# Optimization experiments

Hardware: AMD Instinct MI355X
Metric: run time of the kernel (lower is better)

## Reference

```python
import jax, jax.numpy as jnp
import numpy as np

B, T, C, H, N_LAYER, LAYER_ID = 4, 2048, 1024, 16, 12, 6
N = C // H
Q = 256  # T % 256 == 0 -> chunk size used by the module


def setup_inputs():
    key = jax.random.key(0)
    ks = jax.random.split(key, 9)
    r0 = LAYER_ID / (N_LAYER - 1)
    r1 = 1.0 - LAYER_ID / N_LAYER
    ddd = (jnp.arange(C, dtype=jnp.float32) / C)[None, None, :]
    h = jnp.arange(C, dtype=jnp.float32)
    s = 1.0 / np.sqrt(C)
    return {
        "x": jax.random.normal(ks[0], (B, T, C), jnp.float32),
        "time_maa_x": 1.0 - ddd ** r1,
        "time_maa_w": 1.0 - ddd ** r1,
        "time_maa_k": 1.0 - ddd ** r1,
        "time_maa_v": 1.0 - (ddd ** r1 + 0.3 * r0),
        "time_maa_r": 1.0 - ddd ** (0.5 * r1),
        "maa_w1": jax.random.uniform(ks[1], (C, 4 * 32), jnp.float32, minval=-0.01, maxval=0.01),
        "maa_w2": jax.random.uniform(ks[2], (4, 32, C), jnp.float32, minval=-0.01, maxval=0.01),
        "decay_w1": jax.random.uniform(ks[3], (C, 64), jnp.float32, minval=-0.01, maxval=0.01),
        "decay_w2": jax.random.uniform(ks[4], (64, C), jnp.float32, minval=-0.01, maxval=0.01),
        "time_decay": (-6.0 + 5.0 * (h / (C - 1)) ** (0.7 + 1.3 * r0))[None, None, :],
        "time_faaaa": (r0 * (1.0 - h / (C - 1))).reshape(1, H, 1, 1, N),
        "Wr": jax.random.normal(ks[5], (C, C), jnp.float32) * s,
        "Wk": jax.random.normal(ks[6], (C, C), jnp.float32) * s,
        "Wv": jax.random.normal(ks[7], (C, C), jnp.float32) * s,
        "Wo": jax.random.normal(ks[8], (C, C), jnp.float32) * s,
        "ln_g": jnp.ones((C,), jnp.float32),
        "ln_b": jnp.zeros((C,), jnp.float32),
    }


def _forward(x, time_maa_x, time_maa_w, time_maa_k, time_maa_v, time_maa_r,
             maa_w1, maa_w2, decay_w1, decay_w2, time_decay, time_faaaa,
             Wr, Wk, Wv, Wo, ln_g, ln_b):
    b, t, c = x.shape
    nc = t // Q
    # time_shift: zero-pad one step at front of time axis, drop last step
    xx = jnp.pad(x, ((0, 0), (1, 0), (0, 0)))[:, :-1] - x
    xxx = x + xx * time_maa_x
    m = jnp.tanh(xxx @ maa_w1).reshape(b, t, 4, -1)  # [B,T,4,32]
    m = jnp.einsum('btfd,fdc->fbtc', m, maa_w2)       # [4,B,T,C]
    mw, mk, mv, mr = m[0], m[1], m[2], m[3]
    xw = x + xx * (time_maa_w + mw)
    xk = x + xx * (time_maa_k + mk)
    xv = x + xx * (time_maa_v + mv)
    xr = x + xx * (time_maa_r + mr)
    r = (xr @ Wr).reshape(b, t, H, N).transpose(0, 2, 1, 3)  # [B,H,T,N]
    k = (xk @ Wk).reshape(b, t, H, N).transpose(0, 2, 1, 3)
    v = (xv @ Wv).reshape(b, t, H, N).transpose(0, 2, 1, 3)
    w = time_decay + jnp.tanh(xw @ decay_w1) @ decay_w2      # [B,T,C]
    w = w.reshape(b, t, H, N).transpose(0, 2, 1, 3).mean(axis=-1)  # [B,H,T]
    w_log = -jnp.exp(w)
    wc = w_log.reshape(b, H, nc, Q, 1)
    wc_cum = jnp.cumsum(wc, axis=-2)
    shifted = jnp.pad(wc_cum, ((0, 0), (0, 0), (0, 0), (1, 0), (0, 0)))[..., :-1, :]
    ws_log = wc.sum(axis=-2, keepdims=True)   # [B,H,nc,1,1]
    w_inter = jnp.exp(ws_log - wc_cum)        # [B,H,nc,Q,1]
    w_intra = jnp.exp(wc_cum - wc)            # [B,H,nc,Q,1]
    ws = jnp.exp(ws_log)                      # [B,H,nc,1,1]
    A = shifted - jnp.swapaxes(wc_cum, -1, -2)  # [B,H,nc,Q,Q]
    strict = jnp.tril(jnp.ones((Q, Q), dtype=bool), -1)
    # torch: tril() -> exp() -> tril(-1)  ==  exp on strict-lower, zero elsewhere
    w_mask = jnp.where(strict, jnp.exp(jnp.where(strict, A, 0.0)), 0.0)
    rr = r.reshape(b, H, nc, Q, N)
    kk = k.reshape(b, H, nc, Q, N)
    vv = v.reshape(b, H, nc, Q, N)
    kv = jnp.einsum('bhcqn,bhcqm->bhcnm', kk * w_inter, vv)  # [B,H,nc,N,N]

    def step(state, inp):
        ws_i, kv_i = inp
        return ws_i * state + kv_i, state  # emit state BEFORE update (as in torch loop)

    _, states = jax.lax.scan(step, jnp.zeros((b, H, N, N), x.dtype),
                             (jnp.moveaxis(ws, 2, 0), jnp.moveaxis(kv, 2, 0)))
    states = jnp.moveaxis(states, 0, 2)  # [B,H,nc,N,N]
    inter = jnp.einsum('bhcqn,bhcnm->bhcqm', rr * w_intra, states)
    scores = jnp.einsum('bhcqn,bhckn->bhcqk', rr, kk) * w_mask
    diag = jnp.sum(rr * (time_faaaa * kk), axis=-1)  # [B,H,nc,Q]
    intra = jnp.einsum('bhcqk,bhckm->bhcqm', scores, vv) + diag[..., None] * vv
    y = (inter + intra).reshape(b, H, t, N).transpose(0, 2, 1, 3).reshape(b, t, c)
    mu = y.mean(axis=-1, keepdims=True)
    var = ((y - mu) ** 2).mean(axis=-1, keepdims=True)
    y = (y - mu) / jnp.sqrt(var + 1e-5) * ln_g + ln_b  # ln_x
    return y @ Wo  # output projection (dropout p=0)


def reference(x, time_maa_x, time_maa_w, time_maa_k, time_maa_v, time_maa_r,
              maa_w1, maa_w2, decay_w1, decay_w2, time_decay, time_faaaa,
              Wr, Wk, Wv, Wo, ln_g, ln_b):
    return _forward(x, time_maa_x, time_maa_w, time_maa_k, time_maa_v, time_maa_r,
                    maa_w1, maa_w2, decay_w1, decay_w2, time_decay, time_faaaa,
                    Wr, Wk, Wv, Wo, ln_g, ln_b)
```

## Files before the change

### kernel.cpp

```cpp
#include <hip/hip_runtime.h>
#include <math.h>

#define BB 4
#define TT 2048
#define CC 1024
#define HH 16
#define NN 64
#define QQ 256
#define NCH 8
#define BT 8192

typedef unsigned short u16;
typedef __attribute__((ext_vector_type(8))) short bf16x8;
typedef __attribute__((ext_vector_type(4))) short bf16x4;
typedef __attribute__((ext_vector_type(4))) float f32x4;
typedef __attribute__((ext_vector_type(4))) u16 u16x4;

__device__ inline u16 f2b(float x) {
  union { float f; unsigned u; } v;
  v.f = x;
  unsigned r = v.u + 0x7FFFu + ((v.u >> 16) & 1u);
  return (u16)(r >> 16);
}
__device__ inline float b2f(u16 u) {
  union { unsigned u; float f; } v;
  v.u = ((unsigned)u) << 16;
  return v.f;
}
__device__ inline bf16x8 ldfrag(const u16* p) {
  bf16x4 lo = *(const bf16x4*)p;
  bf16x4 hi = *(const bf16x4*)(p + 4);
  return __builtin_shufflevector(lo, hi, 0, 1, 2, 3, 4, 5, 6, 7);
}
__device__ inline void stage_tile(const u16* __restrict__ g, size_t base,
                                  int pitch, int tid, u16* __restrict__ lds) {
#pragma unroll
  for (int it = 0; it < 2; it++) {
    int cidx = tid + it * 256;
    int r = cidx >> 3, c8 = (cidx & 7) * 8;
    bf16x8 v = *(const bf16x8*)(g + base + (size_t)r * pitch + c8);
    *(bf16x4*)(lds + r * 72 + c8) = __builtin_shufflevector(v, v, 0, 1, 2, 3);
    *(bf16x4*)(lds + r * 72 + c8 + 4) = __builtin_shufflevector(v, v, 4, 5, 6, 7);
  }
}

__global__ __launch_bounds__(256) void mix_kernel(const float* __restrict__ x,
                                                  const float* __restrict__ tmx,
                                                  u16* __restrict__ xxxb) {
  size_t e = ((size_t)blockIdx.x * 256 + threadIdx.x) * 4;
  int c = (int)(e & 1023);
  size_t row = e >> 10;
  int t = (int)(row & 2047);
  float4 xv = *(const float4*)(x + e);
  float4 pv = make_float4(0.f, 0.f, 0.f, 0.f);
  if (t > 0) pv = *(const float4*)(x + e - 1024);
  float4 d = make_float4(pv.x - xv.x, pv.y - xv.y, pv.z - xv.z, pv.w - xv.w);
  u16x4 o;
  o.x = f2b(xv.x + d.x * tmx[c + 0]);
  o.y = f2b(xv.y + d.y * tmx[c + 1]);
  o.z = f2b(xv.z + d.z * tmx[c + 2]);
  o.w = f2b(xv.w + d.w * tmx[c + 3]);
  *(u16x4*)(xxxb + e) = o;
}

__global__ __launch_bounds__(256) void cvt_wT(const float* __restrict__ W0,
                                              const float* __restrict__ W1,
                                              const float* __restrict__ W2,
                                              const float* __restrict__ W3,
                                              u16* __restrict__ O0,
                                              u16* __restrict__ O1,
                                              u16* __restrict__ O2,
                                              u16* __restrict__ O3) {
  const float* W;
  u16* O;
  switch (blockIdx.z) {
    case 0: W = W0; O = O0; break;
    case 1: W = W1; O = O1; break;
    case 2: W = W2; O = O2; break;
    default: W = W3; O = O3; break;
  }
  __shared__ float t[64][65];
  int bx = blockIdx.x * 64;
  int by = blockIdx.y * 64;
#pragma unroll
  for (int it = 0; it < 16; it++) {
    int idx = it * 256 + threadIdx.x;
    int r = idx >> 6, c = idx & 63;
    t[r][c] = W[(size_t)(by + r) * 1024 + bx + c];
  }
  __syncthreads();
#pragma unroll
  for (int it = 0; it < 16; it++) {
    int idx = it * 256 + threadIdx.x;
    int n = idx >> 6, k = idx & 63;
    O[(size_t)(bx + n) * 1024 + by + k] = f2b(t[k][n]);
  }
}

__global__ __launch_bounds__(256) void cvt3_T(const float* __restrict__ w1,
                                              const float* __restrict__ w2,
                                              const float* __restrict__ d1,
                                              u16* __restrict__ o1,
                                              u16* __restrict__ o2,
                                              u16* __restrict__ o3,
                                              const float* __restrict__ dw2,
                                              const float* __restrict__ td,
                                              float* __restrict__ dw2r,
                                              float* __restrict__ tdr,
                                              u16* __restrict__ dw2rbT) {
  if (blockIdx.z == 3) {
    if (blockIdx.y != 0 || blockIdx.x >= 4) return;
    int idx = blockIdx.x * 256 + threadIdx.x;
    if (idx < 1024) {
      int j = idx >> 4, h = idx & 15;
      float s = 0.f;
      for (int n = 0; n < 64; n++) s += dw2[(size_t)j * 1024 + h * 64 + n];
      float m = s * (1.f / 64.f);
      dw2r[j * 16 + h] = m;
      dw2rbT[h * 64 + j] = f2b(m);
    }
    if (idx < 16) {
      float s = 0.f;
      for (int n = 0; n < 64; n++) s += td[idx * 64 + n];
      tdr[idx] = s * (1.f / 64.f);
    }
    return;
  }
  const float* in;
  u16* out;
  int R, C;
  switch (blockIdx.z) {
    case 0: in = w1; out = o1; R = 1024; C = 128; break;
    case 1: in = w2; out = o2; R = 128; C = 1024; break;
    default: in = d1; out = o3; R = 1024; C = 64; break;
  }
  int c0 = blockIdx.x * 64, r0 = blockIdx.y * 64;
  if (c0 >= C || r0 >= R) return;
  __shared__ float t[64][65];
#pragma unroll
  for (int it = 0; it < 16; it++) {
    int idx = it * 256 + threadIdx.x;
    int r = idx >> 6, c = idx & 63;
    t[r][c] = in[(size_t)(r0 + r) * C + c0 + c];
  }
  __syncthreads();
#pragma unroll
  for (int it = 0; it < 16; it++) {
    int idx = it * 256 + threadIdx.x;
    int c = idx >> 6, r = idx & 63;
    out[(size_t)(c0 + c) * R + r0 + r] = f2b(t[r][c]);
  }
}

__global__ __launch_bounds__(256) void gemm_maa(const u16* __restrict__ A,
                                                const u16* __restrict__ Bt,
                                                u16* __restrict__ Cb) {
  __shared__ u16 As[64 * 32];
  __shared__ u16 Bs[64 * 32];
  const int tid = threadIdx.x;
  const int lane = tid & 63;
  const int wave = tid >> 6;
  const int wc = wave * 16;
  const int fr = lane & 15;
  const int fq = lane >> 4;
  const int row0 = blockIdx.y * 64;
  const int col0 = blockIdx.x * 64;

  f32x4 acc[4];
#pragma unroll
  for (int i = 0; i < 4; i++) acc[i] = (f32x4){0.f, 0.f, 0.f, 0.f};

  const int ra = tid >> 2, ca = (tid & 3) * 8;

  for (int k0 = 0; k0 < 1024; k0 += 32) {
    __builtin_amdgcn_global_load_lds(
        (const __attribute__((address_space(1))) void*)(A + (size_t)(row0 + ra) * 1024 + k0 + ca),
        (__attribute__((address_space(3))) void*)(As + tid * 8), 16, 0, 0);
    __builtin_amdgcn_global_load_lds(
        (const __attribute__((address_space(1))) void*)(Bt + (size_t)(col0 + ra) * 1024 + k0 + ca),
        (__attribute__((address_space(3))) void*)(Bs + tid * 8), 16, 0, 0);
    __syncthreads();
    bf16x8 bf = *(const bf16x8*)(Bs + ((wc + fr) * 32 + fq * 8));
#pragma unroll
    for (int i = 0; i < 4; i++) {
      bf16x8 af = *(const bf16x8*)(As + ((i * 16 + fr) * 32 + fq * 8));
      acc[i] = __builtin_amdgcn_mfma_f32_16x16x32_bf16(af, bf, acc[i], 0, 0, 0);
    }
    __syncthreads();
  }
#pragma unroll
  for (int i = 0; i < 4; i++) {
    int grow = row0 + i * 16 + fq * 4;
#pragma unroll
    for (int r = 0; r < 4; r++)
      Cb[(size_t)(grow + r) * 128 + col0 + wc + fr] = f2b(tanhf(acc[i][r]));
  }
}

#define DP_ABUF 8192
#define DP_BBUF 16384
#define DP_SBUF 24576
#define DP_SMEM_BYTES 147456

template <bool TRIPLE, bool F32OUT>
__global__ __launch_bounds__(512, 2) void gemm_dp(
    const u16* __restrict__ A0, const u16* __restrict__ A1,
    const u16* __restrict__ A2, const u16* __restrict__ B0,
    const u16* __restrict__ B1, const u16* __restrict__ B2,
    float* __restrict__ Cf, u16* __restrict__ C0, u16* __restrict__ C1,
    u16* __restrict__ C2) {
  extern __shared__ __align__(16) u16 smem[];
  const int nwg = (int)(gridDim.x * gridDim.y * gridDim.z);
  const int wg = (int)(blockIdx.x + (blockIdx.y << 2) + (blockIdx.z << 8));
  const int cpx = nwg >> 3;
  const int swz = (wg & 7) * cpx + (wg >> 3);
  const int bx = swz & 3;
  const int by = (swz >> 2) & 63;
  const int bz = swz >> 8;

  const u16* __restrict__ A;
  const u16* __restrict__ Bt;
  u16* __restrict__ Cb;
  if (TRIPLE) {
    switch (bz) {
      case 0: A = A0; Bt = B0; Cb = C0; break;
      case 1: A = A1; Bt = B1; Cb = C1; break;
      default: A = A2; Bt = B2; Cb = C2; break;
    }
  } else {
    A = A0; Bt = B0; Cb = C0;
  }

  const int tid = threadIdx.x;
  const int lane = tid & 63;
  const int wave = tid >> 6;
  const int wr = (wave >> 2) * 64;
  const int wc = (wave & 3) * 64;
  const int fr = lane & 15;
  const int fq = lane >> 4;
  const int s8 = fr & 7;
  const int row0 = by * 128;
  const int col0 = bx * 256;

  int aoff[4][2], boff[4][2];
#pragma unroll
  for (int mi = 0; mi < 4; mi++)
#pragma unroll
    for (int ks = 0; ks < 2; ks++)
      aoff[mi][ks] = (wr + mi * 16 + fr) * 64 + (((ks * 4 + fq) ^ s8) * 8);
#pragma unroll
  for (int nj = 0; nj < 4; nj++)
#pragma unroll
    for (int ks = 0; ks < 2; ks++)
      boff[nj][ks] = (wc + nj * 16 + fr) * 64 + (((ks * 4 + fq) ^ s8) * 8);

  auto stage = [&](int kt, int q) {
    const u16* __restrict__ gA = A + (size_t)row0 * 1024 + kt * 64;
    const u16* __restrict__ gB = Bt + (size_t)col0 * 1024 + kt * 64;
    u16* dA = smem + q * DP_SBUF;
    u16* dB = dA + DP_ABUF;
#pragma unroll
    for (int p = 0; p < 2; p++) {
      int pos = tid + p * 512;
      int r = pos >> 3, gch = (pos & 7) ^ (r & 7);
      __builtin_amdgcn_global_load_lds(
          (const __attribute__((address_space(1))) void*)(gA + (size_t)r * 1024 + gch * 8),
          (__attribute__((address_space(3))) void*)(dA + pos * 8), 16, 0, 0);
    }
#pragma unroll
    for (int p = 0; p < 4; p++) {
      int pos = tid + p * 512;
      int r = pos >> 3, gch = (pos & 7) ^ (r & 7);
      __builtin_amdgcn_global_load_lds(
          (const __attribute__((address_space(1))) void*)(gB + (size_t)r * 1024 + gch * 8),
          (__attribute__((address_space(3))) void*)(dB + pos * 8), 16, 0, 0);
    }
  };

  f32x4 acc[4][4];
#pragma unroll
  for (int mi = 0; mi < 4; mi++)
#pragma unroll
    for (int nj = 0; nj < 4; nj++) acc[mi][nj] = (f32x4){0.f, 0.f, 0.f, 0.f};

  auto iter_body = [&](int qc, int qs, bool dostage, int t2) {
    if (dostage) stage(t2, qs);
    const u16* sA = smem + qc * DP_SBUF;
    const u16* sB = sA + DP_ABUF;
    bf16x8 av[4][2], bv[4][2];
#pragma unroll
    for (int mi = 0; mi < 4; mi++)
#pragma unroll
      for (int ks = 0; ks < 2; ks++)
        av[mi][ks] = *(const bf16x8*)(sA + aoff[mi][ks]);
#pragma unroll
    for (int nj = 0; nj < 4; nj++)
#pragma unroll
      for (int ks = 0; ks < 2; ks++)
        bv[nj][ks] = *(const bf16x8*)(sB + boff[nj][ks]);
    __builtin_amdgcn_s_setprio(1);
#pragma unroll
    for (int ks = 0; ks < 2; ks++)
#pragma unroll
      for (int mi = 0; mi < 4; mi++)
#pragma unroll
        for (int nj = 0; nj < 4; nj++)
          acc[mi][nj] = __builtin_amdgcn_mfma_f32_16x16x32_bf16(
              av[mi][ks], bv[nj][ks], acc[mi][nj], 0, 0, 0);
    __builtin_amdgcn_s_setprio(0);
  };

  stage(0, 0);
  stage(1, 1);
  int qc = 0, qs = 2;
  for (int t = 0; t < 14; t++) {
    asm volatile("s_waitcnt vmcnt(6)" ::: "memory");
    __builtin_amdgcn_s_barrier();
    iter_body(qc, qs, true, t + 2);
    qc = (qc == 2) ? 0 : qc + 1;
    qs = (qs == 2) ? 0 : qs + 1;
  }
  asm volatile("s_waitcnt vmcnt(6)" ::: "memory");
  __builtin_amdgcn_s_barrier();
  iter_body(qc, 0, false, 0);
  qc = (qc == 2) ? 0 : qc + 1;
  asm volatile("s_waitcnt vmcnt(0)" ::: "memory");
  __builtin_amdgcn_s_barrier();
  iter_body(qc, 0, false, 0);

#pragma unroll
  for (int mi = 0; mi < 4; mi++) {
    int grow = row0 + wr + mi * 16 + fq * 4;
#pragma unroll
    for (int nj = 0; nj < 4; nj++) {
      int gcol = col0 + wc + nj * 16 + fr;
#pragma unroll
      for (int r = 0; r < 4; r++) {
        if (F32OUT)
          Cf[(size_t)(grow + r) * 1024 + gcol] = acc[mi][nj][r];
        else
          Cb[(size_t)(grow + r) * 1024 + gcol] = f2b(acc[mi][nj][r]);
      }
    }
  }
}

__global__ __launch_bounds__(256) void blend_mfma(
    const u16* __restrict__ mb, const u16* __restrict__ w2T,
    const float* __restrict__ x,
    const float* __restrict__ tmw, const float* __restrict__ tmk,
    const float* __restrict__ tmv, const float* __restrict__ tmr,
    u16* __restrict__ xwb, u16* __restrict__ xkb, u16* __restrict__ xvb,
    u16* __restrict__ xrb) {
  __shared__ u16 mS[64 * 136];
  __shared__ u16 wS[64 * 136];
  const int tid = threadIdx.x;
  const int lane = tid & 63;
  const int w = tid >> 6;
  const int fr = lane & 15;
  const int fq = lane >> 4;
  const int c0 = blockIdx.x * 64;
  const int bt0 = blockIdx.y * 64;

#pragma unroll
  for (int it = 0; it < 4; it++) {
    int idx = tid + it * 256;
    int r = idx >> 4, c8 = (idx & 15) * 8;
    bf16x8 v = *(const bf16x8*)(mb + (size_t)(bt0 + r) * 128 + c8);
    *(bf16x4*)(mS + r * 136 + c8) = __builtin_shufflevector(v, v, 0, 1, 2, 3);
    *(bf16x4*)(mS + r * 136 + c8 + 4) = __builtin_shufflevector(v, v, 4, 5, 6, 7);
    bf16x8 u = *(const bf16x8*)(w2T + (size_t)(c0 + r) * 128 + c8);
    *(bf16x4*)(wS + r * 136 + c8) = __builtin_shufflevector(u, u, 0, 1, 2, 3);
    *(bf16x4*)(wS + r * 136 + c8 + 4) = __builtin_shufflevector(u, u, 4, 5, 6, 7);
  }
  __syncthreads();

  f32x4 acc[4][4];
#pragma unroll
  for (int j = 0; j < 4; j++)
#pragma unroll
    for (int f = 0; f < 4; f++) acc[j][f] = (f32x4){0.f, 0.f, 0.f, 0.f};

#pragma unroll
  for (int f = 0; f < 4; f++) {
    bf16x8 aA = ldfrag(mS + (w * 16 + fr) * 136 + f * 32 + fq * 8);
#pragma unroll
    for (int j = 0; j < 4; j++) {
      bf16x8 bB = ldfrag(wS + (j * 16 + fr) * 136 + f * 32 + fq * 8);
      acc[j][f] = __builtin_amdgcn_mfma_f32_16x16x32_bf16(aA, bB, acc[j][f], 0, 0, 0);
    }
  }

#pragma unroll
  for (int j = 0; j < 4; j++) {
    int c = c0 + j * 16 + fr;
    float w_ = tmw[c], k_ = tmk[c], v_ = tmv[c], r_ = tmr[c];
#pragma unroll
    for (int rr = 0; rr < 4; rr++) {
      int bt = bt0 + w * 16 + fq * 4 + rr;
      size_t g = (size_t)bt * 1024 + c;
      float xv_ = x[g];
      float xp = ((bt & 2047) != 0) ? x[g - 1024] : 0.f;
      float dx = xp - xv_;
      xwb[g] = f2b(xv_ + dx * (w_ + acc[j][0][rr]));
      xkb[g] = f2b(xv_ + dx * (k_ + acc[j][1][rr]));
      xvb[g] = f2b(xv_ + dx * (v_ + acc[j][2][rr]));
      xrb[g] = f2b(xv_ + dx * (r_ + acc[j][3][rr]));
    }
  }
}

__global__ __launch_bounds__(256) void decay_mfma(const u16* __restrict__ xwb,
                                                  const u16* __restrict__ d1T,
                                                  const u16* __restrict__ dw2rbT,
                                                  const float* __restrict__ tdr,
                                                  float* __restrict__ wlog) {
  __shared__ u16 As[64 * 32];
  __shared__ u16 Bs[64 * 32];
  __shared__ u16 h1S[64 * 72];
  __shared__ u16 dwS[16 * 72];
  const int tid = threadIdx.x;
  const int lane = tid & 63;
  const int w = tid >> 6;
  const int fr = lane & 15;
  const int fq = lane >> 4;
  const int bt0 = blockIdx.x * 64;

#pragma unroll
  for (int it = 0; it < 4; it++) {
    int idx = tid + it * 256;
    int r = idx >> 6, c = idx & 63;
    dwS[r * 72 + c] = dw2rbT[r * 64 + c];
  }

  f32x4 acc[4];
#pragma unroll
  for (int j = 0; j < 4; j++) acc[j] = (f32x4){0.f, 0.f, 0.f, 0.f};

  const int ra = tid >> 2, ca = (tid & 3) * 8;
  for (int k0 = 0; k0 < 1024; k0 += 32) {
    __builtin_amdgcn_global_load_lds(
        (const __attribute__((address_space(1))) void*)(xwb + (size_t)(bt0 + ra) * 1024 + k0 + ca),
        (__attribute__((address_space(3))) void*)(As + tid * 8), 16, 0, 0);
    __builtin_amdgcn_global_load_lds(
        (const __attribute__((address_space(1))) void*)(d1T + (size_t)ra * 1024 + k0 + ca),
        (__attribute__((address_space(3))) void*)(Bs + tid * 8), 16, 0, 0);
    __syncthreads();
    bf16x8 aA = *(const bf16x8*)(As + ((w * 16 + fr) * 32 + fq * 8));
#pragma unroll
    for (int j = 0; j < 4; j++) {
      bf16x8 bB = *(const bf16x8*)(Bs + ((j * 16 + fr) * 32 + fq * 8));
      acc[j] = __builtin_amdgcn_mfma_f32_16x16x32_bf16(aA, bB, acc[j], 0, 0, 0);
    }
    __syncthreads();
  }
#pragma unroll
  for (int j = 0; j < 4; j++)
#pragma unroll
    for (int rr = 0; rr < 4; rr++)
      h1S[(w * 16 + fq * 4 + rr) * 72 + j * 16 + fr] = f2b(tanhf(acc[j][rr]));
  __syncthreads();

  f32x4 a2 = (f32x4){0.f, 0.f, 0.f, 0.f};
#pragma unroll
  for (int ks = 0; ks < 2; ks++) {
    bf16x8 aA = ldfrag(h1S + (w * 16 + fr) * 72 + ks * 32 + fq * 8);
    bf16x8 bB = ldfrag(dwS + fr * 72 + ks * 32 + fq * 8);
    a2 = __builtin_amdgcn_mfma_f32_16x16x32_bf16(aA, bB, a2, 0, 0, 0);
  }
  float tdv = tdr[fr];
#pragma unroll
  for (int rr = 0; rr < 4; rr++) {
    int bt = bt0 + w * 16 + fq * 4 + rr;
    int b = bt >> 11, tl = bt & 2047;
    wlog[((size_t)(b * 16 + fr)) * 2048 + tl] = -__expf(tdv + a2[rr]);
  }
}

__global__ __launch_bounds__(256) void wprep_kernel(const float* __restrict__ wlog,
                                                    float* __restrict__ cum,
                                                    float* __restrict__ excl,
                                                    float* __restrict__ wsl) {
  int bid = blockIdx.x;
  int c = bid & 7, bh = bid >> 3;
  int q = threadIdx.x;
  float v = wlog[(size_t)bh * 2048 + c * 256 + q];
  __shared__ float s[256];
  s[q] = v;
  float val = v;
  for (int off = 1; off < 256; off <<= 1) {
    __syncthreads();
    float t = (q >= off) ? s[q - off] : 0.f;
    __syncthreads();
    val += t;
    s[q] = val;
  }
  __syncthreads();
  float total = s[255];
  cum[(size_t)bid * 256 + q] = val;
  excl[(size_t)bid * 256 + q] = val - v;
  if (q == 0) wsl[bid] = total;
}

__global__ __launch_bounds__(256) void kvfuse_kernel(
    const u16* __restrict__ vb, const u16* __restrict__ kb,
    const u16* __restrict__ rb, const float* __restrict__ faaaa,
    const float* __restrict__ cum, const float* __restrict__ wsl,
    u16* __restrict__ vT, float* __restrict__ diagG, float* __restrict__ kvb) {
  int bid = blockIdx.x;
  int c = bid & 7, bh = bid >> 3;
  int b = bh >> 4, h = bh & 15;
  __shared__ float tv[64][65];
  __shared__ float tk[64][65];
  __shared__ u16 kSb[64 * 72];
  __shared__ u16 vSb[64 * 72];
  __shared__ float wfacS[256];
  __shared__ float faS[64];
  const int tid = threadIdx.x;
  const int lane = tid & 63;
  const int w = tid >> 6;
  const int fr = lane & 15;
  const int fq = lane >> 4;
  const int m = lane;

  float wslog = wsl[bid];
  wfacS[tid] = __expf(wslog - cum[(size_t)bid * 256 + tid]);
  if (tid < 64) faS[tid] = faaaa[h * 64 + tid];

  f32x4 acc[4];
#pragma unroll
  for (int j = 0; j < 4; j++) acc[j] = (f32x4){0.f, 0.f, 0.f, 0.f};

  for (int qt = 0; qt < 4; qt++) {
    __syncthreads();
    float fam = faS[m];
    int t0 = c * QQ + qt * 64;
#pragma unroll
    for (int it = 0; it < 16; it++) {
      int r = it * 4 + w;
      size_t g = ((size_t)(b * TT + t0 + r)) * CC + h * 64 + m;
      float vraw = b2f(vb[g]);
      float kraw = b2f(kb[g]);
      float rraw = b2f(rb[g]);
      tv[r][m] = vraw;
      tk[r][m] = kraw;
      float s = rraw * fam * kraw;
      s += __shfl_xor(s, 1);
      s += __shfl_xor(s, 2);
      s += __shfl_xor(s, 4);
      s += __shfl_xor(s, 8);
      s += __shfl_xor(s, 16);
      s += __shfl_xor(s, 32);
      if (m == 0) diagG[(size_t)bh * 2048 + t0 + r] = s;
    }
    __syncthreads();
#pragma unroll
    for (int it = 0; it < 16; it++) {
      int idx = it * 256 + tid;
      int mm = idx >> 6, tl = idx & 63;
      float vv = tv[tl][mm];
      float kk = tk[tl][mm] * wfacS[qt * 64 + tl];
      u16 vbv = f2b(vv);
      vT[((size_t)(bh * 64 + mm)) * TT + t0 + tl] = vbv;
      vSb[mm * 72 + tl] = vbv;
      kSb[mm * 72 + tl] = f2b(kk);
    }
    __syncthreads();
#pragma unroll
    for (int ks = 0; ks < 2; ks++) {
      bf16x8 aA = ldfrag(kSb + (w * 16 + fr) * 72 + ks * 32 + fq * 8);
#pragma unroll
      for (int j = 0; j < 4; j++) {
        bf16x8 bB = ldfrag(vSb + (j * 16 + fr) * 72 + ks * 32 + fq * 8);
        acc[j] = __builtin_amdgcn_mfma_f32_16x16x32_bf16(aA, bB, acc[j], 0, 0, 0);
      }
    }
  }
#pragma unroll
  for (int j = 0; j < 4; j++)
#pragma unroll
    for (int rr = 0; rr < 4; rr++)
      kvb[(size_t)bid * 4096 + (w * 16 + fq * 4 + rr) * 64 + j * 16 + fr] = acc[j][rr];
}

__global__ __launch_bounds__(256) void scan_kernel(const float* __restrict__ kvb,
                                                   const float* __restrict__ wsl,
                                                   float* __restrict__ st) {
  int bh = blockIdx.x >> 2;
  int sl = blockIdx.x & 3;
  int tid = threadIdx.x;
  float s[4];
#pragma unroll
  for (int i = 0; i < 4; i++) s[i] = 0.f;
  for (int c = 0; c < 8; c++) {
    int bid = bh * 8 + c;
    float w = __expf(wsl[bid]);
#pragma unroll
    for (int i = 0; i < 4; i++) {
      size_t e = (size_t)bid * 4096 + sl * 1024 + i * 256 + tid;
      st[e] = s[i];
      s[i] = w * s[i] + kvb[e];
    }
  }
}

__global__ __launch_bounds__(256) void attn_mfma(
    const u16* __restrict__ rb, const u16* __restrict__ kb,
    const u16* __restrict__ vT, const float* __restrict__ stg,
    const float* __restrict__ cum, const float* __restrict__ excl,
    const float* __restrict__ diagG, float* __restrict__ y) {
  int bid = blockIdx.x;
  int c = bid & 7, bh = bid >> 3;
  int b = bh >> 4, h = bh & 15;
  __shared__ u16 rt[64 * 72];
  __shared__ u16 kt[64 * 72];
  __shared__ u16 vt[64 * 72];
  __shared__ u16 pt[64 * 72];
  __shared__ u16 stT[64 * 72];
  __shared__ float cumS[256], exS[256], diagS[256], ekS[256];

  const int tid = threadIdx.x;
  const int lane = tid & 63;
  const int w = tid >> 6;
  const int fr = lane & 15;
  const int fq = lane >> 4;

  cumS[tid] = cum[(size_t)bid * 256 + tid];
  exS[tid] = excl[(size_t)bid * 256 + tid];
  diagS[tid] = diagG[(size_t)bh * 2048 + c * 256 + tid];
#pragma unroll
  for (int it = 0; it < 16; it++) {
    int idx = tid + it * 256;
    int n = idx >> 6, mm = idx & 63;
    stT[mm * 72 + n] = f2b(stg[(size_t)bid * 4096 + idx]);
  }
  __syncthreads();
  const float ccm = cumS[127];
  ekS[tid] = __expf(ccm - cumS[tid]);

  const size_t rowbase = ((size_t)b * TT + c * QQ) * CC + h * 64;
  const size_t vbase0 = (size_t)bh * 64 * TT + c * QQ;

  for (int qt = 0; qt < 4; qt++) {
    __syncthreads();
    stage_tile(rb, rowbase + (size_t)(qt * 64) * CC, CC, tid, rt);
    __syncthreads();

    f32x4 acc[4];
#pragma unroll
    for (int jm = 0; jm < 4; jm++) acc[jm] = (f32x4){0.f, 0.f, 0.f, 0.f};
    bf16x8 rA[2];
    rA[0] = ldfrag(rt + (w * 16 + fr) * 72 + fq * 8);
    rA[1] = ldfrag(rt + (w * 16 + fr) * 72 + 32 + fq * 8);
#pragma unroll
    for (int ks = 0; ks < 2; ks++)
#pragma unroll
      for (int jm = 0; jm < 4; jm++) {
        bf16x8 bB = ldfrag(stT + (jm * 16 + fr) * 72 + ks * 32 + fq * 8);
        acc[jm] = __builtin_amdgcn_mfma_f32_16x16x32_bf16(rA[ks], bB, acc[jm], 0, 0, 0);
      }
    int ql0 = w * 16 + fq * 4;
    float er[4], eqc[4];
#pragma unroll
    for (int rr = 0; rr < 4; rr++) {
      float ex = exS[qt * 64 + ql0 + rr];
      er[rr] = __expf(ex);
      eqc[rr] = __expf(ex - ccm);
    }
#pragma unroll
    for (int jm = 0; jm < 4; jm++)
#pragma unroll
      for (int rr = 0; rr < 4; rr++) acc[jm][rr] *= er[rr];

    for (int kti = 0; kti <= qt; kti++) {
      __syncthreads();
      stage_tile(kb, rowbase + (size_t)(kti * 64) * CC, CC, tid, kt);
      stage_tile(vT, vbase0 + (size_t)(kti * 64), TT, tid, vt);
      __syncthreads();

      f32x4 sacc[4];
#pragma unroll
      for (int jj = 0; jj < 4; jj++) sacc[jj] = (f32x4){0.f, 0.f, 0.f, 0.f};
#pragma unroll
      for (int ks = 0; ks < 2; ks++)
#pragma unroll
        for (int jj = 0; jj < 4; jj++) {
          bf16x8 bB = ldfrag(kt + (jj * 16 + fr) * 72 + ks * 32 + fq * 8);
          sacc[jj] = __builtin_amdgcn_mfma_f32_16x16x32_bf16(rA[ks], bB, sacc[jj], 0, 0, 0);
        }
#pragma unroll
      for (int jj = 0; jj < 4; jj++) {
        int kcol = kti * 64 + jj * 16 + fr;
        float ek = ekS[kcol];
#pragma unroll
        for (int rr = 0; rr < 4; rr++) {
          int qrow = qt * 64 + ql0 + rr;
          float vsc;
          if (kcol < qrow)
            vsc = sacc[jj][rr] * eqc[rr] * ek;
          else if (kcol == qrow)
            vsc = diagS[qrow];
          else
            vsc = 0.f;
          pt[(ql0 + rr) * 72 + jj * 16 + fr] = f2b(vsc);
        }
      }
      __syncthreads();
#pragma unroll
      for (int ks = 0; ks < 2; ks++) {
        bf16x8 pA = ldfrag(pt + (w * 16 + fr) * 72 + ks * 32 + fq * 8);
#pragma unroll
        for (int jm = 0; jm < 4; jm++) {
          bf16x8 vB = ldfrag(vt + (jm * 16 + fr) * 72 + ks * 32 + fq * 8);
          acc[jm] = __builtin_amdgcn_mfma_f32_16x16x32_bf16(pA, vB, acc[jm], 0, 0, 0);
        }
      }
    }
    int qg0 = qt * 64 + w * 16 + fq * 4;
#pragma unroll
    for (int jm = 0; jm < 4; jm++)
#pragma unroll
      for (int rr = 0; rr < 4; rr++)
        y[rowbase + (size_t)(qg0 + rr) * CC + jm * 16 + fr] = acc[jm][rr];
  }
}

__global__ __launch_bounds__(256) void ln_kernel(const float* __restrict__ y,
                                                 const float* __restrict__ g,
                                                 const float* __restrict__ bta,
                                                 u16* __restrict__ out) {
  __shared__ float red[8];
  int bt = blockIdx.x;
  int tid = threadIdx.x;
  float v[4];
  float s = 0.f;
#pragma unroll
  for (int i = 0; i < 4; i++) {
    v[i] = y[(size_t)bt * 1024 + i * 256 + tid];
    s += v[i];
  }
#pragma unroll
  for (int off = 32; off > 0; off >>= 1) s += __shfl_down(s, off);
  if ((tid & 63) == 0) red[tid >> 6] = s;
  __syncthreads();
  if (tid == 0) red[4] = red[0] + red[1] + red[2] + red[3];
  __syncthreads();
  float mu = red[4] * (1.f / 1024.f);
  float s2 = 0.f;
#pragma unroll
  for (int i = 0; i < 4; i++) {
    float d = v[i] - mu;
    s2 += d * d;
  }
#pragma unroll
  for (int off = 32; off > 0; off >>= 1) s2 += __shfl_down(s2, off);
  __syncthreads();
  if ((tid & 63) == 0) red[tid >> 6] = s2;
  __syncthreads();
  if (tid == 0) red[5] = red[0] + red[1] + red[2] + red[3];
  __syncthreads();
  float var = red[5] * (1.f / 1024.f);
  float rstd = rsqrtf(var + 1e-5f);
#pragma unroll
  for (int i = 0; i < 4; i++) {
    int c = i * 256 + tid;
    out[(size_t)bt * 1024 + c] = f2b((v[i] - mu) * rstd * g[c] + bta[c]);
  }
}

extern "C" void kernel_launch(void* const* d_in, const int* in_sizes, int n_in,
                              void* d_out, int out_size, void* d_ws,
                              size_t ws_size, hipStream_t stream) {
  const float* x = (const float*)d_in[0];
  const float* tmx = (const float*)d_in[1];
  const float* tmw = (const float*)d_in[2];
  const float* tmk = (const float*)d_in[3];
  const float* tmv = (const float*)d_in[4];
  const float* tmr = (const float*)d_in[5];
  const float* maa_w1 = (const float*)d_in[6];
  const float* maa_w2 = (const float*)d_in[7];
  const float* decay_w1 = (const float*)d_in[8];
  const float* decay_w2 = (const float*)d_in[9];
  const float* time_decay = (const float*)d_in[10];
  const float* faaaa = (const float*)d_in[11];
  const float* Wr = (const float*)d_in[12];
  const float* Wk = (const float*)d_in[13];
  const float* Wv = (const float*)d_in[14];
  const float* Wo = (const float*)d_in[15];
  const float* lng = (const float*)d_in[16];
  const float* lnb = (const float*)d_in[17];
  float* out = (float*)d_out;
  float* ws = (float*)d_ws;

  const size_t S = (size_t)BT * CC;

  float* y_ = ws;
  float* dw2r = ws + S;
  float* tdr = dw2r + 1024;
  float* wlog = tdr + 1024;
  float* cum = wlog + 131072;
  float* excl = cum + 131072;
  float* wsl = excl + 131072;
  float* diagG = wsl + 1024;
  float* kvb = diagG + 131072;
  float* stb = kvb + (size_t)512 * 4096;
  float* fend = stb + (size_t)512 * 4096;
  u16* xxxb = (u16*)fend;
  u16* mb = xxxb + S;
  u16* xkb = mb + (size_t)BT * 128;
  u16* xvb = xkb + S;
  u16* xrb = xvb + S;
  u16* xwb = xrb + S;
  u16* rb16 = xwb + S;
  u16* kb16 = rb16 + S;
  u16* Vb = kb16 + S;
  u16* Wrt = Vb + S;
  u16* Wkt = Wrt + (size_t)1024 * 1024;
  u16* Wvt = Wkt + (size_t)1024 * 1024;
  u16* Wot = Wvt + (size_t)1024 * 1024;
  u16* w1T = Wot + (size_t)1024 * 1024;
  u16* w2T = w1T + (size_t)128 * 1024;
  u16* d1T = w2T + (size_t)1024 * 128;
  u16* dw2rbT = d1T + (size_t)64 * 1024;
  u16* vT = xxxb;
  u16* ylnb = xkb;

  static bool attr_done = false;
  if (!attr_done) {
    hipFuncSetAttribute((const void*)gemm_dp<true, false>,
                        hipFuncAttributeMaxDynamicSharedMemorySize, DP_SMEM_BYTES);
    hipFuncSetAttribute((const void*)gemm_dp<false, true>,
                        hipFuncAttributeMaxDynamicSharedMemorySize, DP_SMEM_BYTES);
    attr_done = true;
  }

  cvt_wT<<<dim3(16, 16, 4), 256, 0, stream>>>(Wr, Wk, Wv, Wo, Wrt, Wkt, Wvt, Wot);
  cvt3_T<<<dim3(16, 16, 4), 256, 0, stream>>>(maa_w1, maa_w2, decay_w1, w1T,
                                              w2T, d1T, decay_w2, time_decay,
                                              dw2r, tdr, dw2rbT);
  mix_kernel<<<8192, 256, 0, stream>>>(x, tmx, xxxb);
  gemm_maa<<<dim3(2, 128), 256, 0, stream>>>(xxxb, w1T, mb);
  blend_mfma<<<dim3(16, 128), 256, 0, stream>>>(mb, w2T, x, tmw, tmk, tmv, tmr,
                                                xwb, xkb, xvb, xrb);
  decay_mfma<<<128, 256, 0, stream>>>(xwb, d1T, dw2rbT, tdr, wlog);
  wprep_kernel<<<512, 256, 0, stream>>>(wlog, cum, excl, wsl);
  gemm_dp<true, false><<<dim3(4, 64, 3), 512, DP_SMEM_BYTES, stream>>>(
      xrb, xkb, xvb, Wrt, Wkt, Wvt, nullptr, rb16, kb16, Vb);
  kvfuse_kernel<<<512, 256, 0, stream>>>(Vb, kb16, rb16, faaaa, cum, wsl, vT,
                                         diagG, kvb);
  scan_kernel<<<256, 256, 0, stream>>>(kvb, wsl, stb);
  attn_mfma<<<512, 256, 0, stream>>>(rb16, kb16, vT, stb, cum, excl, diagG, y_);
  ln_kernel<<<BT, 256, 0, stream>>>(y_, lng, lnb, ylnb);
  gemm_dp<false, true><<<dim3(4, 64, 1), 512, DP_SMEM_BYTES, stream>>>(
      ylnb, nullptr, nullptr, Wot, nullptr, nullptr, out, nullptr, nullptr,
      nullptr);
}
```

Before: 361.0 us.

## Fuse token-shift mix into maa GEMM and restructure decay, scan, attention, layernorm kernels

Removes the separate mix kernel by computing the time-shift blend inside gemm_maa's A-tile load, avoiding a bf16 intermediate round trip. decay_mfma now uses 32-row blocks with a 64-wide K step and XOR-swizzled LDS layout, doubling the grid. The scan and layernorm kernels use vectorized float4 loads and stores. attn_mfma stages all four r tiles up front in dynamic shared memory and reorders loops so each k/v tile is loaded once for all query tiles, at the cost of more registers and LDS.

```diff
diff --git a/kernel.cpp b/kernel.cpp
--- a/kernel.cpp
+++ b/kernel.cpp
@@ -42,25 +42,6 @@
     *(bf16x4*)(lds + r * 72 + c8) = __builtin_shufflevector(v, v, 0, 1, 2, 3);
     *(bf16x4*)(lds + r * 72 + c8 + 4) = __builtin_shufflevector(v, v, 4, 5, 6, 7);
   }
-}
-
-__global__ __launch_bounds__(256) void mix_kernel(const float* __restrict__ x,
-                                                  const float* __restrict__ tmx,
-                                                  u16* __restrict__ xxxb) {
-  size_t e = ((size_t)blockIdx.x * 256 + threadIdx.x) * 4;
-  int c = (int)(e & 1023);
-  size_t row = e >> 10;
-  int t = (int)(row & 2047);
-  float4 xv = *(const float4*)(x + e);
-  float4 pv = make_float4(0.f, 0.f, 0.f, 0.f);
-  if (t > 0) pv = *(const float4*)(x + e - 1024);
-  float4 d = make_float4(pv.x - xv.x, pv.y - xv.y, pv.z - xv.z, pv.w - xv.w);
-  u16x4 o;
-  o.x = f2b(xv.x + d.x * tmx[c + 0]);
-  o.y = f2b(xv.y + d.y * tmx[c + 1]);
-  o.z = f2b(xv.z + d.z * tmx[c + 2]);
-  o.w = f2b(xv.w + d.w * tmx[c + 3]);
-  *(u16x4*)(xxxb + e) = o;
 }
 
 __global__ __launch_bounds__(256) void cvt_wT(const float* __restrict__ W0,
@@ -152,7 +133,8 @@
   }
 }
 
-__global__ __launch_bounds__(256) void gemm_maa(const u16* __restrict__ A,
+__global__ __launch_bounds__(256) void gemm_maa(const float* __restrict__ x,
+                                                const float* __restrict__ tmx,
                                                 const u16* __restrict__ Bt,
                                                 u16* __restrict__ Cb) {
   __shared__ u16 As[64 * 32];
@@ -171,14 +153,34 @@
   for (int i = 0; i < 4; i++) acc[i] = (f32x4){0.f, 0.f, 0.f, 0.f};
 
   const int ra = tid >> 2, ca = (tid & 3) * 8;
+  const int bt = row0 + ra;
+  const bool hasprev = ((bt & 2047) != 0);
 
   for (int k0 = 0; k0 < 1024; k0 += 32) {
-    __builtin_amdgcn_global_load_lds(
-        (const __attribute__((address_space(1))) void*)(A + (size_t)(row0 + ra) * 1024 + k0 + ca),
-        (__attribute__((address_space(3))) void*)(As + tid * 8), 16, 0, 0);
     __builtin_amdgcn_global_load_lds(
         (const __attribute__((address_space(1))) void*)(Bt + (size_t)(col0 + ra) * 1024 + k0 + ca),
         (__attribute__((address_space(3))) void*)(Bs + tid * 8), 16, 0, 0);
+    float4 xa = *(const float4*)(x + (size_t)bt * 1024 + k0 + ca);
+    float4 xb = *(const float4*)(x + (size_t)bt * 1024 + k0 + ca + 4);
+    float4 pa = make_float4(0.f, 0.f, 0.f, 0.f);
+    float4 pb = make_float4(0.f, 0.f, 0.f, 0.f);
+    if (hasprev) {
+      pa = *(const float4*)(x + (size_t)(bt - 1) * 1024 + k0 + ca);
+      pb = *(const float4*)(x + (size_t)(bt - 1) * 1024 + k0 + ca + 4);
+    }
+    float4 ta = *(const float4*)(tmx + k0 + ca);
+    float4 tb = *(const float4*)(tmx + k0 + ca + 4);
+    u16x4 oa, ob;
+    oa.x = f2b(xa.x + (pa.x - xa.x) * ta.x);
+    oa.y = f2b(xa.y + (pa.y - xa.y) * ta.y);
+    oa.z = f2b(xa.z + (pa.z - xa.z) * ta.z);
+    oa.w = f2b(xa.w + (pa.w - xa.w) * ta.w);
+    ob.x = f2b(xb.x + (pb.x - xb.x) * tb.x);
+    ob.y = f2b(xb.y + (pb.y - xb.y) * tb.y);
+    ob.z = f2b(xb.z + (pb.z - xb.z) * tb.z);
+    ob.w = f2b(xb.w + (pb.w - xb.w) * tb.w);
+    *(u16x4*)(As + tid * 8) = oa;
+    *(u16x4*)(As + tid * 8 + 4) = ob;
     __syncthreads();
     bf16x8 bf = *(const bf16x8*)(Bs + ((wc + fr) * 32 + fq * 8));
 #pragma unroll
@@ -415,16 +417,17 @@
                                                   const u16* __restrict__ dw2rbT,
                                                   const float* __restrict__ tdr,
                                                   float* __restrict__ wlog) {
-  __shared__ u16 As[64 * 32];
-  __shared__ u16 Bs[64 * 32];
-  __shared__ u16 h1S[64 * 72];
+  __shared__ u16 As[32 * 64];
+  __shared__ u16 Bs[64 * 64];
+  __shared__ u16 h1S[32 * 72];
   __shared__ u16 dwS[16 * 72];
   const int tid = threadIdx.x;
   const int lane = tid & 63;
   const int w = tid >> 6;
   const int fr = lane & 15;
   const int fq = lane >> 4;
-  const int bt0 = blockIdx.x * 64;
+  const int s8 = fr & 7;
+  const int bt0 = blockIdx.x * 32;
 
 #pragma unroll
   for (int it = 0; it < 4; it++) {
@@ -433,47 +436,62 @@
     dwS[r * 72 + c] = dw2rbT[r * 64 + c];
   }
 
-  f32x4 acc[4];
-#pragma unroll
-  for (int j = 0; j < 4; j++) acc[j] = (f32x4){0.f, 0.f, 0.f, 0.f};
-
-  const int ra = tid >> 2, ca = (tid & 3) * 8;
-  for (int k0 = 0; k0 < 1024; k0 += 32) {
+  f32x4 acc[2];
+#pragma unroll
+  for (int mi = 0; mi < 2; mi++) acc[mi] = (f32x4){0.f, 0.f, 0.f, 0.f};
+
+  const int raA = tid >> 3;
+  const int gchA = (tid & 7) ^ (raA & 7);
+
+  for (int k0 = 0; k0 < 1024; k0 += 64) {
     __builtin_amdgcn_global_load_lds(
-        (const __attribute__((address_space(1))) void*)(xwb + (size_t)(bt0 + ra) * 1024 + k0 + ca),
+        (const __attribute__((address_space(1))) void*)(
+            xwb + (size_t)(bt0 + raA) * 1024 + k0 + gchA * 8),
         (__attribute__((address_space(3))) void*)(As + tid * 8), 16, 0, 0);
-    __builtin_amdgcn_global_load_lds(
-        (const __attribute__((address_space(1))) void*)(d1T + (size_t)ra * 1024 + k0 + ca),
-        (__attribute__((address_space(3))) void*)(Bs + tid * 8), 16, 0, 0);
-    __syncthreads();
-    bf16x8 aA = *(const bf16x8*)(As + ((w * 16 + fr) * 32 + fq * 8));
-#pragma unroll
-    for (int j = 0; j < 4; j++) {
-      bf16x8 bB = *(const bf16x8*)(Bs + ((j * 16 + fr) * 32 + fq * 8));
-      acc[j] = __builtin_amdgcn_mfma_f32_16x16x32_bf16(aA, bB, acc[j], 0, 0, 0);
-    }
-    __syncthreads();
-  }
-#pragma unroll
-  for (int j = 0; j < 4; j++)
+#pragma unroll
+    for (int p = 0; p < 2; p++) {
+      int pos = tid + p * 256;
+      int r = pos >> 3, gch = (pos & 7) ^ (r & 7);
+      __builtin_amdgcn_global_load_lds(
+          (const __attribute__((address_space(1))) void*)(
+              d1T + (size_t)r * 1024 + k0 + gch * 8),
+          (__attribute__((address_space(3))) void*)(Bs + pos * 8), 16, 0, 0);
+    }
+    __syncthreads();
+#pragma unroll
+    for (int ks = 0; ks < 2; ks++) {
+      int chunk = ((ks * 4 + fq) ^ s8) * 8;
+      bf16x8 bB = *(const bf16x8*)(Bs + (w * 16 + fr) * 64 + chunk);
+#pragma unroll
+      for (int mi = 0; mi < 2; mi++) {
+        bf16x8 aA = *(const bf16x8*)(As + (mi * 16 + fr) * 64 + chunk);
+        acc[mi] = __builtin_amdgcn_mfma_f32_16x16x32_bf16(aA, bB, acc[mi], 0, 0, 0);
+      }
+    }
+    __syncthreads();
+  }
+#pragma unroll
+  for (int mi = 0; mi < 2; mi++)
 #pragma unroll
     for (int rr = 0; rr < 4; rr++)
-      h1S[(w * 16 + fq * 4 + rr) * 72 + j * 16 + fr] = f2b(tanhf(acc[j][rr]));
-  __syncthreads();
-
-  f32x4 a2 = (f32x4){0.f, 0.f, 0.f, 0.f};
-#pragma unroll
-  for (int ks = 0; ks < 2; ks++) {
-    bf16x8 aA = ldfrag(h1S + (w * 16 + fr) * 72 + ks * 32 + fq * 8);
-    bf16x8 bB = ldfrag(dwS + fr * 72 + ks * 32 + fq * 8);
-    a2 = __builtin_amdgcn_mfma_f32_16x16x32_bf16(aA, bB, a2, 0, 0, 0);
-  }
-  float tdv = tdr[fr];
-#pragma unroll
-  for (int rr = 0; rr < 4; rr++) {
-    int bt = bt0 + w * 16 + fq * 4 + rr;
-    int b = bt >> 11, tl = bt & 2047;
-    wlog[((size_t)(b * 16 + fr)) * 2048 + tl] = -__expf(tdv + a2[rr]);
+      h1S[(mi * 16 + fq * 4 + rr) * 72 + w * 16 + fr] = f2b(tanhf(acc[mi][rr]));
+  __syncthreads();
+
+  if (w < 2) {
+    f32x4 a2 = (f32x4){0.f, 0.f, 0.f, 0.f};
+#pragma unroll
+    for (int ks = 0; ks < 2; ks++) {
+      bf16x8 aA = ldfrag(h1S + (w * 16 + fr) * 72 + ks * 32 + fq * 8);
+      bf16x8 bB = ldfrag(dwS + fr * 72 + ks * 32 + fq * 8);
+      a2 = __builtin_amdgcn_mfma_f32_16x16x32_bf16(aA, bB, a2, 0, 0, 0);
+    }
+    float tdv = tdr[fr];
+#pragma unroll
+    for (int rr = 0; rr < 4; rr++) {
+      int bt = bt0 + w * 16 + fq * 4 + rr;
+      int b = bt >> 11, tl = bt & 2047;
+      wlog[((size_t)(b * 16 + fr)) * 2048 + tl] = -__expf(tdv + a2[rr]);
+    }
   }
 }
 
@@ -589,36 +607,39 @@
   int bh = blockIdx.x >> 2;
   int sl = blockIdx.x & 3;
   int tid = threadIdx.x;
-  float s[4];
-#pragma unroll
-  for (int i = 0; i < 4; i++) s[i] = 0.f;
+  f32x4 s = (f32x4){0.f, 0.f, 0.f, 0.f};
   for (int c = 0; c < 8; c++) {
     int bid = bh * 8 + c;
     float w = __expf(wsl[bid]);
-#pragma unroll
-    for (int i = 0; i < 4; i++) {
-      size_t e = (size_t)bid * 4096 + sl * 1024 + i * 256 + tid;
-      st[e] = s[i];
-      s[i] = w * s[i] + kvb[e];
-    }
-  }
-}
+    size_t e = (size_t)bid * 4096 + sl * 1024 + tid * 4;
+    f32x4 kv = *(const f32x4*)(kvb + e);
+    *(f32x4*)(st + e) = s;
+    s = w * s + kv;
+  }
+}
+
+#define AT_T 4608
+#define AT_SMEM_BYTES 77824
 
 __global__ __launch_bounds__(256) void attn_mfma(
     const u16* __restrict__ rb, const u16* __restrict__ kb,
     const u16* __restrict__ vT, const float* __restrict__ stg,
     const float* __restrict__ cum, const float* __restrict__ excl,
     const float* __restrict__ diagG, float* __restrict__ y) {
+  extern __shared__ __align__(16) u16 asmem[];
+  u16* rt = asmem;
+  u16* kt = rt + 4 * AT_T;
+  u16* vt = kt + AT_T;
+  u16* pt = vt + AT_T;
+  u16* stT = pt + AT_T;
+  float* cumS = (float*)(stT + AT_T);
+  float* exS = cumS + 256;
+  float* diagS = exS + 256;
+  float* ekS = diagS + 256;
+
   int bid = blockIdx.x;
   int c = bid & 7, bh = bid >> 3;
   int b = bh >> 4, h = bh & 15;
-  __shared__ u16 rt[64 * 72];
-  __shared__ u16 kt[64 * 72];
-  __shared__ u16 vt[64 * 72];
-  __shared__ u16 pt[64 * 72];
-  __shared__ u16 stT[64 * 72];
-  __shared__ float cumS[256], exS[256], diagS[256], ekS[256];
-
   const int tid = threadIdx.x;
   const int lane = tid & 63;
   const int w = tid >> 6;
@@ -634,50 +655,54 @@
     int n = idx >> 6, mm = idx & 63;
     stT[mm * 72 + n] = f2b(stg[(size_t)bid * 4096 + idx]);
   }
+  const size_t rowbase = ((size_t)b * TT + c * QQ) * CC + h * 64;
+  const size_t vbase0 = (size_t)bh * 64 * TT + c * QQ;
+#pragma unroll
+  for (int qt = 0; qt < 4; qt++)
+    stage_tile(rb, rowbase + (size_t)(qt * 64) * CC, CC, tid, rt + qt * AT_T);
   __syncthreads();
   const float ccm = cumS[127];
   ekS[tid] = __expf(ccm - cumS[tid]);
 
-  const size_t rowbase = ((size_t)b * TT + c * QQ) * CC + h * 64;
-  const size_t vbase0 = (size_t)bh * 64 * TT + c * QQ;
-
+  const int ql0 = w * 16 + fq * 4;
+  bf16x8 rA[4][2];
+  f32x4 acc[4][4];
+  float eqc[4][4];
+#pragma unroll
   for (int qt = 0; qt < 4; qt++) {
-    __syncthreads();
-    stage_tile(rb, rowbase + (size_t)(qt * 64) * CC, CC, tid, rt);
-    __syncthreads();
-
-    f32x4 acc[4];
-#pragma unroll
-    for (int jm = 0; jm < 4; jm++) acc[jm] = (f32x4){0.f, 0.f, 0.f, 0.f};
-    bf16x8 rA[2];
-    rA[0] = ldfrag(rt + (w * 16 + fr) * 72 + fq * 8);
-    rA[1] = ldfrag(rt + (w * 16 + fr) * 72 + 32 + fq * 8);
+    rA[qt][0] = ldfrag(rt + qt * AT_T + (w * 16 + fr) * 72 + fq * 8);
+    rA[qt][1] = ldfrag(rt + qt * AT_T + (w * 16 + fr) * 72 + 32 + fq * 8);
+#pragma unroll
+    for (int jm = 0; jm < 4; jm++) acc[qt][jm] = (f32x4){0.f, 0.f, 0.f, 0.f};
 #pragma unroll
     for (int ks = 0; ks < 2; ks++)
 #pragma unroll
       for (int jm = 0; jm < 4; jm++) {
         bf16x8 bB = ldfrag(stT + (jm * 16 + fr) * 72 + ks * 32 + fq * 8);
-        acc[jm] = __builtin_amdgcn_mfma_f32_16x16x32_bf16(rA[ks], bB, acc[jm], 0, 0, 0);
+        acc[qt][jm] = __builtin_amdgcn_mfma_f32_16x16x32_bf16(rA[qt][ks], bB,
+                                                             acc[qt][jm], 0, 0, 0);
       }
-    int ql0 = w * 16 + fq * 4;
-    float er[4], eqc[4];
+    float er[4];
 #pragma unroll
     for (int rr = 0; rr < 4; rr++) {
       float ex = exS[qt * 64 + ql0 + rr];
       er[rr] = __expf(ex);
-      eqc[rr] = __expf(ex - ccm);
+      eqc[qt][rr] = __expf(ex - ccm);
     }
 #pragma unroll
     for (int jm = 0; jm < 4; jm++)
 #pragma unroll
-      for (int rr = 0; rr < 4; rr++) acc[jm][rr] *= er[rr];
-
-    for (int kti = 0; kti <= qt; kti++) {
-      __syncthreads();
-      stage_tile(kb, rowbase + (size_t)(kti * 64) * CC, CC, tid, kt);
-      stage_tile(vT, vbase0 + (size_t)(kti * 64), TT, tid, vt);
-      __syncthreads();
-
+      for (int rr = 0; rr < 4; rr++) acc[qt][jm][rr] *= er[rr];
+  }
+
+#pragma unroll
+  for (int kti = 0; kti < 4; kti++) {
+    __syncthreads();
+    stage_tile(kb, rowbase + (size_t)(kti * 64) * CC, CC, tid, kt);
+    stage_tile(vT, vbase0 + (size_t)(kti * 64), TT, tid, vt);
+    __syncthreads();
+#pragma unroll
+    for (int qt = kti; qt < 4; qt++) {
       f32x4 sacc[4];
 #pragma unroll
       for (int jj = 0; jj < 4; jj++) sacc[jj] = (f32x4){0.f, 0.f, 0.f, 0.f};
@@ -686,7 +711,8 @@
 #pragma unroll
         for (int jj = 0; jj < 4; jj++) {
           bf16x8 bB = ldfrag(kt + (jj * 16 + fr) * 72 + ks * 32 + fq * 8);
-          sacc[jj] = __builtin_amdgcn_mfma_f32_16x16x32_bf16(rA[ks], bB, sacc[jj], 0, 0, 0);
+          sacc[jj] = __builtin_amdgcn_mfma_f32_16x16x32_bf16(rA[qt][ks], bB,
+                                                             sacc[jj], 0, 0, 0);
         }
 #pragma unroll
       for (int jj = 0; jj < 4; jj++) {
@@ -697,7 +723,7 @@
           int qrow = qt * 64 + ql0 + rr;
           float vsc;
           if (kcol < qrow)
-            vsc = sacc[jj][rr] * eqc[rr] * ek;
+            vsc = sacc[jj][rr] * eqc[qt][rr] * ek;
           else if (kcol == qrow)
             vsc = diagS[qrow];
           else
@@ -712,16 +738,21 @@
 #pragma unroll
         for (int jm = 0; jm < 4; jm++) {
           bf16x8 vB = ldfrag(vt + (jm * 16 + fr) * 72 + ks * 32 + fq * 8);
-          acc[jm] = __builtin_amdgcn_mfma_f32_16x16x32_bf16(pA, vB, acc[jm], 0, 0, 0);
+          acc[qt][jm] = __builtin_amdgcn_mfma_f32_16x16x32_bf16(pA, vB,
+                                                               acc[qt][jm], 0, 0, 0);
         }
       }
-    }
-    int qg0 = qt * 64 + w * 16 + fq * 4;
+      __syncthreads();
+    }
+  }
+#pragma unroll
+  for (int qt = 0; qt < 4; qt++) {
+    int qg0 = qt * 64 + ql0;
 #pragma unroll
     for (int jm = 0; jm < 4; jm++)
 #pragma unroll
       for (int rr = 0; rr < 4; rr++)
-        y[rowbase + (size_t)(qg0 + rr) * CC + jm * 16 + fr] = acc[jm][rr];
+        y[rowbase + (size_t)(qg0 + rr) * CC + jm * 16 + fr] = acc[qt][jm][rr];
   }
 }
 
@@ -732,13 +763,8 @@
   __shared__ float red[8];
   int bt = blockIdx.x;
   int tid = threadIdx.x;
-  float v[4];
-  float s = 0.f;
-#pragma unroll
-  for (int i = 0; i < 4; i++) {
-    v[i] = y[(size_t)bt * 1024 + i * 256 + tid];
-    s += v[i];
-  }
+  float4 v = *(const float4*)(y + (size_t)bt * 1024 + tid * 4);
+  float s = v.x + v.y + v.z + v.w;
 #pragma unroll
   for (int off = 32; off > 0; off >>= 1) s += __shfl_down(s, off);
   if ((tid & 63) == 0) red[tid >> 6] = s;
@@ -746,12 +772,8 @@
   if (tid == 0) red[4] = red[0] + red[1] + red[2] + red[3];
   __syncthreads();
   float mu = red[4] * (1.f / 1024.f);
-  float s2 = 0.f;
-#pragma unroll
-  for (int i = 0; i < 4; i++) {
-    float d = v[i] - mu;
-    s2 += d * d;
-  }
+  float d0 = v.x - mu, d1 = v.y - mu, d2 = v.z - mu, d3 = v.w - mu;
+  float s2 = d0 * d0 + d1 * d1 + d2 * d2 + d3 * d3;
 #pragma unroll
   for (int off = 32; off > 0; off >>= 1) s2 += __shfl_down(s2, off);
   __syncthreads();
@@ -761,11 +783,14 @@
   __syncthreads();
   float var = red[5] * (1.f / 1024.f);
   float rstd = rsqrtf(var + 1e-5f);
-#pragma unroll
-  for (int i = 0; i < 4; i++) {
-    int c = i * 256 + tid;
-    out[(size_t)bt * 1024 + c] = f2b((v[i] - mu) * rstd * g[c] + bta[c]);
-  }
+  float4 g4 = *(const float4*)(g + tid * 4);
+  float4 b4 = *(const float4*)(bta + tid * 4);
+  u16x4 o;
+  o.x = f2b(d0 * rstd * g4.x + b4.x);
+  o.y = f2b(d1 * rstd * g4.y + b4.y);
+  o.z = f2b(d2 * rstd * g4.z + b4.z);
+  o.w = f2b(d3 * rstd * g4.w + b4.w);
+  *(u16x4*)(out + (size_t)bt * 1024 + tid * 4) = o;
 }
 
 extern "C" void kernel_launch(void* const* d_in, const int* in_sizes, int n_in,
@@ -831,6 +856,8 @@
                         hipFuncAttributeMaxDynamicSharedMemorySize, DP_SMEM_BYTES);
     hipFuncSetAttribute((const void*)gemm_dp<false, true>,
                         hipFuncAttributeMaxDynamicSharedMemorySize, DP_SMEM_BYTES);
+    hipFuncSetAttribute((const void*)attn_mfma,
+                        hipFuncAttributeMaxDynamicSharedMemorySize, AT_SMEM_BYTES);
     attr_done = true;
   }
 
@@ -838,18 +865,18 @@
   cvt3_T<<<dim3(16, 16, 4), 256, 0, stream>>>(maa_w1, maa_w2, decay_w1, w1T,
                                               w2T, d1T, decay_w2, time_decay,
                                               dw2r, tdr, dw2rbT);
-  mix_kernel<<<8192, 256, 0, stream>>>(x, tmx, xxxb);
-  gemm_maa<<<dim3(2, 128), 256, 0, stream>>>(xxxb, w1T, mb);
+  gemm_maa<<<dim3(2, 128), 256, 0, stream>>>(x, tmx, w1T, mb);
   blend_mfma<<<dim3(16, 128), 256, 0, stream>>>(mb, w2T, x, tmw, tmk, tmv, tmr,
                                                 xwb, xkb, xvb, xrb);
-  decay_mfma<<<128, 256, 0, stream>>>(xwb, d1T, dw2rbT, tdr, wlog);
+  decay_mfma<<<256, 256, 0, stream>>>(xwb, d1T, dw2rbT, tdr, wlog);
   wprep_kernel<<<512, 256, 0, stream>>>(wlog, cum, excl, wsl);
   gemm_dp<true, false><<<dim3(4, 64, 3), 512, DP_SMEM_BYTES, stream>>>(
       xrb, xkb, xvb, Wrt, Wkt, Wvt, nullptr, rb16, kb16, Vb);
   kvfuse_kernel<<<512, 256, 0, stream>>>(Vb, kb16, rb16, faaaa, cum, wsl, vT,
                                          diagG, kvb);
   scan_kernel<<<256, 256, 0, stream>>>(kvb, wsl, stb);
-  attn_mfma<<<512, 256, 0, stream>>>(rb16, kb16, vT, stb, cum, excl, diagG, y_);
+  attn_mfma<<<512, 256, AT_SMEM_BYTES, stream>>>(rb16, kb16, vT, stb, cum, excl,
+                                                 diagG, y_);
   ln_kernel<<<BT, 256, 0, stream>>>(y_, lng, lnb, ylnb);
   gemm_dp<false, true><<<dim3(4, 64, 1), 512, DP_SMEM_BYTES, stream>>>(
       ylnb, nullptr, nullptr, Wot, nullptr, nullptr, out, nullptr, nullptr,
```

Result: slower. 371.0 us (+2.8%).
